# Optimization experiments

Measured on AMD Instinct MI355X. Metric: run time of the kernel, lower is better.

Reference implementation:

```python
import jax, jax.numpy as jnp
import numpy as np

B, D, C, Q = 4096, 128, 1000, 65536
PROTO_M = 0.99
EPS = 1e-12


def _l2norm(x, axis=-1):
    n = jnp.sqrt(jnp.sum(x * x, axis=axis, keepdims=True))
    return x / jnp.maximum(n, EPS)


def setup_inputs() -> dict:
    key = jax.random.key(0)
    ks = jax.random.split(key, 7)
    q = _l2norm(jax.random.normal(ks[0], (B, D), dtype=jnp.float32))
    k = _l2norm(jax.random.normal(ks[1], (B, D), dtype=jnp.float32))
    classfy_logits = jax.random.normal(ks[2], (B, C), dtype=jnp.float32)
    plabel = jax.random.uniform(ks[3], (B, C), dtype=jnp.float32)
    prototypes = _l2norm(jax.random.normal(ks[4], (C, D), dtype=jnp.float32))
    queue = _l2norm(jax.random.normal(ks[5], (Q, D), dtype=jnp.float32))
    queue_pseudo = jax.random.randint(ks[6], (Q,), 0, C).astype(jnp.float32)
    return {
        "q": q, "k": k, "classfy_logits": classfy_logits, "plabel": plabel,
        "prototypes": prototypes, "queue": queue, "queue_pseudo": queue_pseudo,
        "ptr": 0,
    }


def reference(q, k, classfy_logits, plabel, prototypes, queue, queue_pseudo, ptr):
    m = PROTO_M
    # classifier softmax (encoder head output)
    classfy_out = jax.nn.softmax(classfy_logits, axis=1)          # [B, C]
    # cluster logits against OLD prototypes (mm happens before EMA update)
    logits_prot = jnp.matmul(q, prototypes.T)                     # [B, C]
    cluster_out = jax.nn.softmax(logits_prot, axis=1)
    # pseudo labels from partial-label-masked scores
    pseudo_labels = jnp.argmax(classfy_out * plabel, axis=1)      # [B] int
    # --- vectorized order-dependent scatter-EMA prototype update ---
    # sequential: proto[l_i] = m*proto[l_i] + (1-m)*q_i  for i = 0..B-1
    # closed form: proto[c]*m^{n_c} + sum_i (1-m)*m^{(#later samples with same label)} q_i
    onehot = (pseudo_labels[:, None] == jnp.arange(C)[None, :])   # [B, C] bool
    counts = jnp.sum(onehot, axis=0)                              # [C] n_c
    rank = jnp.take_along_axis(jnp.cumsum(onehot.astype(jnp.int32), axis=0),
                               pseudo_labels[:, None], axis=1)[:, 0] - 1  # [B]
    n_l = counts[pseudo_labels]                                   # [B]
    w = (1.0 - m) * jnp.power(jnp.float32(m), (n_l - 1 - rank).astype(jnp.float32))
    scatter = jnp.zeros_like(prototypes).at[pseudo_labels].add(w[:, None] * q)
    decay = jnp.power(jnp.float32(m), counts.astype(jnp.float32))[:, None]
    new_prototypes = _l2norm(prototypes * decay + scatter, axis=1)
    # --- MoCo queue enqueue/dequeue (contrastive bank uses OLD queue) ---
    cont_features = jnp.concatenate([q, k, queue], axis=0)        # [2B+Q, D]
    pl_f = pseudo_labels.astype(jnp.float32)
    cont_labels = jnp.concatenate([pl_f, pl_f, queue_pseudo], axis=0)
    new_queue = jax.lax.dynamic_update_slice(queue, k, (ptr, 0))
    new_queue_pseudo = jax.lax.dynamic_update_slice(queue_pseudo, pl_f, (ptr,))
    new_ptr = (ptr + q.shape[0]) % queue.shape[0]
    return (classfy_out, cluster_out, cont_features, cont_labels,
            new_prototypes, new_queue, new_queue_pseudo, new_ptr)
```

## Files before the change

kernel.cpp:

```cpp
#include <hip/hip_runtime.h>
#include <hip/hip_bf16.h>
#include <math.h>

#define Bn 4096
#define Dn 128
#define Cn 1000
#define Qn 65536

typedef __attribute__((ext_vector_type(8))) short short8v;
typedef __attribute__((ext_vector_type(4))) short short4v;
typedef __attribute__((ext_vector_type(4))) float f32x4;
typedef __attribute__((ext_vector_type(4))) float f4v;

__device__ inline float waveAllMaxF(float v) {
    for (int o = 32; o; o >>= 1) v = fmaxf(v, __shfl_xor(v, o));
    return v;
}
__device__ inline float waveAllSumF(float v) {
    for (int o = 32; o; o >>= 1) v += __shfl_xor(v, o);
    return v;
}
__device__ inline float waveSumF(float v) {
    for (int o = 32; o; o >>= 1) v += __shfl_down(v, o);
    return v;
}
__device__ inline short f2bf(float x) {
    union { __hip_bfloat16 h; short s; } u;
    u.h = __float2bfloat16(x);
    return u.s;
}

__global__ __launch_bounds__(256) void k_cls(
    const float* __restrict__ logits, const float* __restrict__ plabel,
    const float* __restrict__ q, const float* __restrict__ proto,
    float* __restrict__ out_cls, int* __restrict__ labels,
    __hip_bfloat16* __restrict__ qb, __hip_bfloat16* __restrict__ pb)
{
    int g = blockIdx.x, t = threadIdx.x;

    if (t < 160) {
        int idx4 = g * 160 + t;
        if (idx4 < 131072) {
            f4v v = *(const f4v*)(q + (long long)idx4 * 4);
            short4v o = {f2bf(v.x), f2bf(v.y), f2bf(v.z), f2bf(v.w)};
            *(short4v*)((short*)qb + (long long)idx4 * 4) = o;
        } else {
            int j4 = idx4 - 131072;
            short4v o = {0, 0, 0, 0};
            if (j4 < 32000) {
                f4v v = *(const f4v*)(proto + (long long)j4 * 4);
                o = (short4v){f2bf(v.x), f2bf(v.y), f2bf(v.z), f2bf(v.w)};
            }
            *(short4v*)((short*)pb + (long long)j4 * 4) = o;
        }
    }

    int lane = t & 63, wid = t >> 6;
    int row = g * 4 + wid;
    const float* x  = logits + (long long)row * Cn;
    const float* pl = plabel + (long long)row * Cn;

    f4v lv[4], pv[4];
#pragma unroll
    for (int j = 0; j < 4; ++j) {
        int f4i = lane + j * 64;
        if (f4i < 250) {
            lv[j] = *(const f4v*)(x + f4i * 4);
            pv[j] = *(const f4v*)(pl + f4i * 4);
        } else {
            lv[j] = (f4v){-INFINITY, -INFINITY, -INFINITY, -INFINITY};
            pv[j] = (f4v){0.f, 0.f, 0.f, 0.f};
        }
    }

    float mx = -INFINITY;
#pragma unroll
    for (int j = 0; j < 4; ++j)
        mx = fmaxf(mx, fmaxf(fmaxf(lv[j].x, lv[j].y), fmaxf(lv[j].z, lv[j].w)));
    mx = waveAllMaxF(mx);

    float vv[16];
    float ssum = 0.f;
#pragma unroll
    for (int j = 0; j < 4; ++j) {
        vv[j * 4 + 0] = expf(lv[j].x - mx);
        vv[j * 4 + 1] = expf(lv[j].y - mx);
        vv[j * 4 + 2] = expf(lv[j].z - mx);
        vv[j * 4 + 3] = expf(lv[j].w - mx);
        ssum += vv[j * 4 + 0] + vv[j * 4 + 1] + vv[j * 4 + 2] + vv[j * 4 + 3];
    }
    ssum = waveAllSumF(ssum);
    float inv = 1.f / ssum;

    float bv = -INFINITY; int bi = Cn;
#pragma unroll
    for (int j = 0; j < 4; ++j) {
        int f4i = lane + j * 64;
        if (f4i < 250) {
            float o0 = vv[j * 4 + 0] * inv, o1 = vv[j * 4 + 1] * inv;
            float o2 = vv[j * 4 + 2] * inv, o3 = vv[j * 4 + 3] * inv;
            *((f4v*)(out_cls + (long long)row * Cn) + f4i) = (f4v){o0, o1, o2, o3};
            float pr[4] = {o0 * pv[j].x, o1 * pv[j].y, o2 * pv[j].z, o3 * pv[j].w};
#pragma unroll
            for (int jj = 0; jj < 4; ++jj) {
                if (pr[jj] > bv) { bv = pr[jj]; bi = f4i * 4 + jj; }
            }
        }
    }
    for (int o = 32; o; o >>= 1) {
        float ov = __shfl_xor(bv, o);
        int   oi = __shfl_xor(bi, o);
        if (ov > bv || (ov == bv && oi < bi)) { bv = ov; bi = oi; }
    }
    if (lane == 0) labels[row] = bi;
}

__global__ __launch_bounds__(256) void k_rest(
    const __hip_bfloat16* __restrict__ qb, const __hip_bfloat16* __restrict__ pbuf,
    const float* __restrict__ proto, const float* __restrict__ q,
    const float* __restrict__ kk, const float* __restrict__ queue,
    const int* __restrict__ lbl, const float* __restrict__ qps,
    const int* __restrict__ ptrp,
    float* __restrict__ outC, float* __restrict__ outp,
    float* __restrict__ out_lab, float* __restrict__ out_qps,
    float* __restrict__ out_ptr,
    float* __restrict__ out_feat, float* __restrict__ out_queue)
{
    __shared__ __align__(16) char smem[32800];
    int bid = blockIdx.x, t = threadIdx.x;

    if (bid < 256) {
        const float* src = (bid < 128) ? q : kk;
        long long sb = (long long)(bid & 127) * 4096;
        long long db = (long long)bid * 4096;
        f4v v[4];
#pragma unroll
        for (int u = 0; u < 4; ++u)
            v[u] = *(const f4v*)(src + sb + (u * 256 + t) * 4);
#pragma unroll
        for (int u = 0; u < 4; ++u)
            *(f4v*)(out_feat + db + (u * 256 + t) * 4) = v[u];
        return;
    }
    if (bid < 2304) {
        int cb = bid - 256;
        int p = *ptrp;
        int pc = p < 0 ? 0 : (p > Qn - Bn ? Qn - Bn : p);
        long long base = (long long)cb * 4096;
        const long long FB = 2LL * Bn * Dn;
        f4v v[4];
#pragma unroll
        for (int u = 0; u < 4; ++u)
            v[u] = *(const f4v*)(queue + base + (u * 256 + t) * 4);
#pragma unroll
        for (int u = 0; u < 4; ++u)
            *(f4v*)(out_feat + FB + base + (u * 256 + t) * 4) = v[u];
#pragma unroll
        for (int u = 0; u < 4; ++u) {
            long long foff = base + (u * 256 + t) * 4;
            int row = (int)(foff >> 7);
            unsigned rr = (unsigned)(row - pc);
            f4v w = v[u];
            if (rr < (unsigned)Bn) w = *(const f4v*)(kk + (long long)rr * Dn + (foff & 127));
            *(f4v*)(out_queue + foff) = w;
        }
        return;
    }

    if (bid < 2560) {
        int gb = bid - 2304;
        float (*red)[4] = (float (*)[4])smem;
        int lane = t & 63, w = t >> 6;
        int la = lane & 15, lk = lane >> 4;
        int row0 = gb * 16;

        f32x4 acc[16];
#pragma unroll
        for (int j = 0; j < 16; ++j) acc[j] = (f32x4){0.f, 0.f, 0.f, 0.f};

        const short* A = (const short*)qb + (long long)(row0 + la) * Dn;
        const short* Bp = (const short*)pbuf;
#pragma unroll
        for (int kc = 0; kc < Dn; kc += 32) {
            short8v a = *(const short8v*)(A + kc + lk * 8);
#pragma unroll
            for (int j = 0; j < 16; ++j) {
                int prow = w * 256 + j * 16 + la;
                short8v b = *(const short8v*)(Bp + (long long)prow * Dn + kc + lk * 8);
                acc[j] = __builtin_amdgcn_mfma_f32_16x16x32_bf16(a, b, acc[j], 0, 0, 0);
            }
        }

        float m[4];
#pragma unroll
        for (int rg = 0; rg < 4; ++rg) {
            float v = -INFINITY;
#pragma unroll
            for (int j = 0; j < 16; ++j) {
                int col = w * 256 + j * 16 + la;
                if (col < Cn) v = fmaxf(v, acc[j][rg]);
            }
#pragma unroll
            for (int o = 1; o < 16; o <<= 1) v = fmaxf(v, __shfl_xor(v, o));
            m[rg] = v;
        }
        if (la == 0) {
#pragma unroll
            for (int rg = 0; rg < 4; ++rg) red[lk * 4 + rg][w] = m[rg];
        }
        __syncthreads();
#pragma unroll
        for (int rg = 0; rg < 4; ++rg) {
            int r = lk * 4 + rg;
            m[rg] = fmaxf(fmaxf(red[r][0], red[r][1]), fmaxf(red[r][2], red[r][3]));
        }
        __syncthreads();

        float s[4];
#pragma unroll
        for (int rg = 0; rg < 4; ++rg) {
            float v = 0.f;
#pragma unroll
            for (int j = 0; j < 16; ++j) {
                int col = w * 256 + j * 16 + la;
                float e = (col < Cn) ? expf(acc[j][rg] - m[rg]) : 0.f;
                acc[j][rg] = e;
                v += e;
            }
#pragma unroll
            for (int o = 1; o < 16; o <<= 1) v += __shfl_xor(v, o);
            s[rg] = v;
        }
        if (la == 0) {
#pragma unroll
            for (int rg = 0; rg < 4; ++rg) red[lk * 4 + rg][w] = s[rg];
        }
        __syncthreads();
#pragma unroll
        for (int rg = 0; rg < 4; ++rg) {
            int r = lk * 4 + rg;
            s[rg] = 1.f / (red[r][0] + red[r][1] + red[r][2] + red[r][3]);
        }

#pragma unroll
        for (int j = 0; j < 16; ++j) {
            int col = w * 256 + j * 16 + la;
            if (col < Cn) {
                int rowb = row0 + lk * 4;
#pragma unroll
                for (int rg = 0; rg < 4; ++rg)
                    outC[(long long)(rowb + rg) * Cn + col] = acc[j][rg] * s[rg];
            }
        }
    } else if (bid < 3060) {
        int* sl = (int*)smem;
        unsigned short* list0 = (unsigned short*)(smem + 16384);
        unsigned short* list1 = list0 + 4096;
        int* nm = (int*)(smem + 32768);
        float* shh = (float*)(smem + 32776);

        int h = t >> 7, tt = t & 127;
        int c = (bid - 2560) * 2 + h;

#pragma unroll
        for (int u = 0; u < 4; ++u) {
            int base = (u * 256 + t) * 4;
            *(int4*)(sl + base) = *(const int4*)(lbl + base);
        }
        if (t == 0)   nm[0] = 0;
        if (t == 128) nm[1] = 0;
        __syncthreads();

        int wv = t >> 6;
        if ((wv & 1) == 0) {
            int hh = wv >> 1;
            int ln = t & 63;
            int cc = (bid - 2560) * 2 + hh;
            unsigned short* lst = hh ? list1 : list0;
            int n = 0;
            for (int jj = 0; jj < Bn / 64; ++jj) {
                unsigned long long mask = __ballot(sl[jj * 64 + ln] == cc);
                if (ln == 0) {
                    while (mask) {
                        int b = __builtin_ctzll(mask);
                        lst[n++] = (unsigned short)(jj * 64 + b);
                        mask &= mask - 1;
                    }
                }
            }
            if (ln == 0) nm[hh] = n;
        }
        __syncthreads();

        int n = nm[h];
        unsigned short* lst = h ? list1 : list0;
        float acc = proto[(long long)c * Dn + tt] * __powf(0.99f, (float)n);
#pragma unroll 4
        for (int mi = 0; mi < n; ++mi)
            acc += 0.01f * __powf(0.99f, (float)(n - 1 - mi)) * q[(long long)lst[mi] * Dn + tt];

        float ss = waveSumF(acc * acc);
        if ((t & 63) == 0) shh[t >> 6] = ss;
        __syncthreads();
        float nn = sqrtf(shh[h * 2] + shh[h * 2 + 1]);
        outp[(long long)c * Dn + tt] = acc / fmaxf(nn, 1e-12f);
    } else {
        int gid = (bid - 3060) * 256 + t;
        const int NL = 2 * Bn + Qn;
        int p = *ptrp;
        int pc = p < 0 ? 0 : (p > Qn - Bn ? Qn - Bn : p);
        if (gid < NL) {
            float v;
            if (gid < Bn)          v = (float)lbl[gid];
            else if (gid < 2 * Bn) v = (float)lbl[gid - Bn];
            else                   v = qps[gid - 2 * Bn];
            out_lab[gid] = v;
        }
        int j = gid - NL;
        if (j >= 0 && j < Qn) {
            unsigned rr = (unsigned)(j - pc);
            out_qps[j] = (rr < (unsigned)Bn) ? (float)lbl[rr] : qps[j];
        }
        if (gid == NL + Qn) out_ptr[0] = (float)((p + Bn) % Qn);
    }
}

extern "C" void kernel_launch(void* const* d_in, const int* in_sizes, int n_in,
                              void* d_out, int out_size, void* d_ws, size_t ws_size,
                              hipStream_t stream)
{
    const float* q     = (const float*)d_in[0];
    const float* kk    = (const float*)d_in[1];
    const float* cl    = (const float*)d_in[2];
    const float* plab  = (const float*)d_in[3];
    const float* proto = (const float*)d_in[4];
    const float* queue = (const float*)d_in[5];
    const float* qps   = (const float*)d_in[6];
    const int*   ptrp  = (const int*)d_in[7];

    float* out = (float*)d_out;
    const long long O_CLU  = 4096000;
    const long long O_FEAT = 8192000;
    const long long O_LAB  = 17629184;
    const long long O_PROT = 17702912;
    const long long O_QUE  = 17830912;
    const long long O_QPS  = 26219520;
    const long long O_PTR  = 26285056;

    char* ws = (char*)d_ws;
    int*   lbl = (int*)(ws + 0);
    __hip_bfloat16* qb = (__hip_bfloat16*)(ws + 1048576);
    __hip_bfloat16* pb = (__hip_bfloat16*)(ws + 2097152);

    k_cls<<<1024, 256, 0, stream>>>(cl, plab, q, proto, out, lbl, qb, pb);
    k_rest<<<3605, 256, 0, stream>>>(qb, pb, proto, q, kk, queue, lbl, qps, ptrp,
                                     out + O_CLU, out + O_PROT,
                                     out + O_LAB, out + O_QPS, out + O_PTR,
                                     out + O_FEAT, out + O_QUE);
}
```

Baseline: 51.85 us.

## Move prototype matmul-softmax into first kernel with inline bf16 conversion

The cluster matmul+softmax no longer depends on labels, so it moves into the first kernel and converts q and prototypes from fp32 to bf16 inline instead of staging them through workspace buffers. The second kernel now runs one block per class for the prototype EMA, building the per-class index list with a parallel ballot/popcount compaction across all four waves instead of a serial lane-0 loop. The memory copies are reordered to run after the prototype blocks. The trade-off is redundant fp32 loads and conversions of prototypes in every matmul block, and more blocks in the second kernel.

```diff
diff --git a/kernel.cpp b/kernel.cpp
--- a/kernel.cpp
+++ b/kernel.cpp
@@ -8,9 +8,9 @@
 #define Qn 65536
 
 typedef __attribute__((ext_vector_type(8))) short short8v;
-typedef __attribute__((ext_vector_type(4))) short short4v;
 typedef __attribute__((ext_vector_type(4))) float f32x4;
 typedef __attribute__((ext_vector_type(4))) float f4v;
+typedef unsigned short ushortT;
 
 __device__ inline float waveAllMaxF(float v) {
     for (int o = 32; o; o >>= 1) v = fmaxf(v, __shfl_xor(v, o));
@@ -30,31 +30,114 @@
     return u.s;
 }
 
-__global__ __launch_bounds__(256) void k_cls(
+__global__ __launch_bounds__(256) void k_one(
     const float* __restrict__ logits, const float* __restrict__ plabel,
     const float* __restrict__ q, const float* __restrict__ proto,
     float* __restrict__ out_cls, int* __restrict__ labels,
-    __hip_bfloat16* __restrict__ qb, __hip_bfloat16* __restrict__ pb)
+    float* __restrict__ outC)
 {
-    int g = blockIdx.x, t = threadIdx.x;
-
-    if (t < 160) {
-        int idx4 = g * 160 + t;
-        if (idx4 < 131072) {
-            f4v v = *(const f4v*)(q + (long long)idx4 * 4);
-            short4v o = {f2bf(v.x), f2bf(v.y), f2bf(v.z), f2bf(v.w)};
-            *(short4v*)((short*)qb + (long long)idx4 * 4) = o;
-        } else {
-            int j4 = idx4 - 131072;
-            short4v o = {0, 0, 0, 0};
-            if (j4 < 32000) {
-                f4v v = *(const f4v*)(proto + (long long)j4 * 4);
-                o = (short4v){f2bf(v.x), f2bf(v.y), f2bf(v.z), f2bf(v.w)};
-            }
-            *(short4v*)((short*)pb + (long long)j4 * 4) = o;
-        }
-    }
-
+    __shared__ float red[16][4];
+    int bid = blockIdx.x, t = threadIdx.x;
+
+    if (bid < 256) {
+        int lane = t & 63, w = t >> 6;
+        int la = lane & 15, lk = lane >> 4;
+        int row0 = bid * 16;
+
+        f32x4 acc[16];
+#pragma unroll
+        for (int j = 0; j < 16; ++j) acc[j] = (f32x4){0.f, 0.f, 0.f, 0.f};
+
+        const float* A0 = q + (long long)(row0 + la) * Dn;
+#pragma unroll
+        for (int kc = 0; kc < Dn; kc += 32) {
+            short8v a;
+            {
+                f4v f0 = *(const f4v*)(A0 + kc + lk * 8);
+                f4v f1 = *(const f4v*)(A0 + kc + lk * 8 + 4);
+                a[0] = f2bf(f0.x); a[1] = f2bf(f0.y); a[2] = f2bf(f0.z); a[3] = f2bf(f0.w);
+                a[4] = f2bf(f1.x); a[5] = f2bf(f1.y); a[6] = f2bf(f1.z); a[7] = f2bf(f1.w);
+            }
+#pragma unroll
+            for (int j = 0; j < 16; ++j) {
+                int prow = w * 256 + j * 16 + la;
+                short8v b = {0, 0, 0, 0, 0, 0, 0, 0};
+                if (prow < Cn) {
+                    const float* Bp0 = proto + (long long)prow * Dn + kc + lk * 8;
+                    f4v f0 = *(const f4v*)Bp0;
+                    f4v f1 = *(const f4v*)(Bp0 + 4);
+                    b[0] = f2bf(f0.x); b[1] = f2bf(f0.y); b[2] = f2bf(f0.z); b[3] = f2bf(f0.w);
+                    b[4] = f2bf(f1.x); b[5] = f2bf(f1.y); b[6] = f2bf(f1.z); b[7] = f2bf(f1.w);
+                }
+                acc[j] = __builtin_amdgcn_mfma_f32_16x16x32_bf16(a, b, acc[j], 0, 0, 0);
+            }
+        }
+
+        float m[4];
+#pragma unroll
+        for (int rg = 0; rg < 4; ++rg) {
+            float v = -INFINITY;
+#pragma unroll
+            for (int j = 0; j < 16; ++j) {
+                int col = w * 256 + j * 16 + la;
+                if (col < Cn) v = fmaxf(v, acc[j][rg]);
+            }
+#pragma unroll
+            for (int o = 1; o < 16; o <<= 1) v = fmaxf(v, __shfl_xor(v, o));
+            m[rg] = v;
+        }
+        if (la == 0) {
+#pragma unroll
+            for (int rg = 0; rg < 4; ++rg) red[lk * 4 + rg][w] = m[rg];
+        }
+        __syncthreads();
+#pragma unroll
+        for (int rg = 0; rg < 4; ++rg) {
+            int r = lk * 4 + rg;
+            m[rg] = fmaxf(fmaxf(red[r][0], red[r][1]), fmaxf(red[r][2], red[r][3]));
+        }
+        __syncthreads();
+
+        float s[4];
+#pragma unroll
+        for (int rg = 0; rg < 4; ++rg) {
+            float v = 0.f;
+#pragma unroll
+            for (int j = 0; j < 16; ++j) {
+                int col = w * 256 + j * 16 + la;
+                float e = (col < Cn) ? expf(acc[j][rg] - m[rg]) : 0.f;
+                acc[j][rg] = e;
+                v += e;
+            }
+#pragma unroll
+            for (int o = 1; o < 16; o <<= 1) v += __shfl_xor(v, o);
+            s[rg] = v;
+        }
+        if (la == 0) {
+#pragma unroll
+            for (int rg = 0; rg < 4; ++rg) red[lk * 4 + rg][w] = s[rg];
+        }
+        __syncthreads();
+#pragma unroll
+        for (int rg = 0; rg < 4; ++rg) {
+            int r = lk * 4 + rg;
+            s[rg] = 1.f / (red[r][0] + red[r][1] + red[r][2] + red[r][3]);
+        }
+
+#pragma unroll
+        for (int j = 0; j < 16; ++j) {
+            int col = w * 256 + j * 16 + la;
+            if (col < Cn) {
+                int rowb = row0 + lk * 4;
+#pragma unroll
+                for (int rg = 0; rg < 4; ++rg)
+                    outC[(long long)(rowb + rg) * Cn + col] = acc[j][rg] * s[rg];
+            }
+        }
+        return;
+    }
+
+    int g = bid - 256;
     int lane = t & 63, wid = t >> 6;
     int row = g * 4 + wid;
     const float* x  = logits + (long long)row * Cn;
@@ -115,197 +198,76 @@
     if (lane == 0) labels[row] = bi;
 }
 
-__global__ __launch_bounds__(256) void k_rest(
-    const __hip_bfloat16* __restrict__ qb, const __hip_bfloat16* __restrict__ pbuf,
+__global__ __launch_bounds__(256) void k_two(
     const float* __restrict__ proto, const float* __restrict__ q,
     const float* __restrict__ kk, const float* __restrict__ queue,
     const int* __restrict__ lbl, const float* __restrict__ qps,
     const int* __restrict__ ptrp,
-    float* __restrict__ outC, float* __restrict__ outp,
+    float* __restrict__ outp,
     float* __restrict__ out_lab, float* __restrict__ out_qps,
     float* __restrict__ out_ptr,
     float* __restrict__ out_feat, float* __restrict__ out_queue)
 {
-    __shared__ __align__(16) char smem[32800];
+    __shared__ ushortT slab[Bn];
+    __shared__ ushortT lists[4][1024];
+    __shared__ int cnts[4];
+    __shared__ float shh[2];
     int bid = blockIdx.x, t = threadIdx.x;
 
-    if (bid < 256) {
-        const float* src = (bid < 128) ? q : kk;
-        long long sb = (long long)(bid & 127) * 4096;
-        long long db = (long long)bid * 4096;
-        f4v v[4];
-#pragma unroll
-        for (int u = 0; u < 4; ++u)
-            v[u] = *(const f4v*)(src + sb + (u * 256 + t) * 4);
-#pragma unroll
-        for (int u = 0; u < 4; ++u)
-            *(f4v*)(out_feat + db + (u * 256 + t) * 4) = v[u];
+    if (bid < 1000) {
+        int c = bid;
+#pragma unroll
+        for (int u = 0; u < 4; ++u) {
+            int4 v = ((const int4*)lbl)[u * 256 + t];
+            int base = (u * 256 + t) * 4;
+            slab[base + 0] = (ushortT)v.x; slab[base + 1] = (ushortT)v.y;
+            slab[base + 2] = (ushortT)v.z; slab[base + 3] = (ushortT)v.w;
+        }
+        __syncthreads();
+
+        int w = t >> 6, ln = t & 63;
+        int cnt = 0;
+        for (int jj = 0; jj < 16; ++jj) {
+            int j = w * 1024 + jj * 64 + ln;
+            bool mt = (slab[j] == (ushortT)c);
+            unsigned long long mask = __ballot(mt);
+            if (mt) {
+                int pos = cnt + __popcll(mask & ((1ull << ln) - 1ull));
+                lists[w][pos] = (ushortT)j;
+            }
+            cnt += (int)__popcll(mask);
+        }
+        if (ln == 0) cnts[w] = cnt;
+        __syncthreads();
+
+        float acc = 0.f;
+        if (t < Dn) {
+            int n = cnts[0] + cnts[1] + cnts[2] + cnts[3];
+            acc = proto[(long long)c * Dn + t] * __powf(0.99f, (float)n);
+            int base = 0;
+#pragma unroll 1
+            for (int w2 = 0; w2 < 4; ++w2) {
+                int cw = cnts[w2];
+                for (int mi = 0; mi < cw; ++mi) {
+                    int r = lists[w2][mi];
+                    acc += 0.01f * __powf(0.99f, (float)(n - 1 - (base + mi)))
+                         * q[(long long)r * Dn + t];
+                }
+                base += cw;
+            }
+        }
+        float ss = waveSumF(acc * acc);
+        if ((t & 63) == 0 && t < Dn) shh[t >> 6] = ss;
+        __syncthreads();
+        if (t < Dn) {
+            float nrm = sqrtf(shh[0] + shh[1]);
+            outp[(long long)c * Dn + t] = acc / fmaxf(nrm, 1e-12f);
+        }
         return;
     }
-    if (bid < 2304) {
-        int cb = bid - 256;
-        int p = *ptrp;
-        int pc = p < 0 ? 0 : (p > Qn - Bn ? Qn - Bn : p);
-        long long base = (long long)cb * 4096;
-        const long long FB = 2LL * Bn * Dn;
-        f4v v[4];
-#pragma unroll
-        for (int u = 0; u < 4; ++u)
-            v[u] = *(const f4v*)(queue + base + (u * 256 + t) * 4);
-#pragma unroll
-        for (int u = 0; u < 4; ++u)
-            *(f4v*)(out_feat + FB + base + (u * 256 + t) * 4) = v[u];
-#pragma unroll
-        for (int u = 0; u < 4; ++u) {
-            long long foff = base + (u * 256 + t) * 4;
-            int row = (int)(foff >> 7);
-            unsigned rr = (unsigned)(row - pc);
-            f4v w = v[u];
-            if (rr < (unsigned)Bn) w = *(const f4v*)(kk + (long long)rr * Dn + (foff & 127));
-            *(f4v*)(out_queue + foff) = w;
-        }
-        return;
-    }
-
-    if (bid < 2560) {
-        int gb = bid - 2304;
-        float (*red)[4] = (float (*)[4])smem;
-        int lane = t & 63, w = t >> 6;
-        int la = lane & 15, lk = lane >> 4;
-        int row0 = gb * 16;
-
-        f32x4 acc[16];
-#pragma unroll
-        for (int j = 0; j < 16; ++j) acc[j] = (f32x4){0.f, 0.f, 0.f, 0.f};
-
-        const short* A = (const short*)qb + (long long)(row0 + la) * Dn;
-        const short* Bp = (const short*)pbuf;
-#pragma unroll
-        for (int kc = 0; kc < Dn; kc += 32) {
-            short8v a = *(const short8v*)(A + kc + lk * 8);
-#pragma unroll
-            for (int j = 0; j < 16; ++j) {
-                int prow = w * 256 + j * 16 + la;
-                short8v b = *(const short8v*)(Bp + (long long)prow * Dn + kc + lk * 8);
-                acc[j] = __builtin_amdgcn_mfma_f32_16x16x32_bf16(a, b, acc[j], 0, 0, 0);
-            }
-        }
-
-        float m[4];
-#pragma unroll
-        for (int rg = 0; rg < 4; ++rg) {
-            float v = -INFINITY;
-#pragma unroll
-            for (int j = 0; j < 16; ++j) {
-                int col = w * 256 + j * 16 + la;
-                if (col < Cn) v = fmaxf(v, acc[j][rg]);
-            }
-#pragma unroll
-            for (int o = 1; o < 16; o <<= 1) v = fmaxf(v, __shfl_xor(v, o));
-            m[rg] = v;
-        }
-        if (la == 0) {
-#pragma unroll
-            for (int rg = 0; rg < 4; ++rg) red[lk * 4 + rg][w] = m[rg];
-        }
-        __syncthreads();
-#pragma unroll
-        for (int rg = 0; rg < 4; ++rg) {
-            int r = lk * 4 + rg;
-            m[rg] = fmaxf(fmaxf(red[r][0], red[r][1]), fmaxf(red[r][2], red[r][3]));
-        }
-        __syncthreads();
-
-        float s[4];
-#pragma unroll
-        for (int rg = 0; rg < 4; ++rg) {
-            float v = 0.f;
-#pragma unroll
-            for (int j = 0; j < 16; ++j) {
-                int col = w * 256 + j * 16 + la;
-                float e = (col < Cn) ? expf(acc[j][rg] - m[rg]) : 0.f;
-                acc[j][rg] = e;
-                v += e;
-            }
-#pragma unroll
-            for (int o = 1; o < 16; o <<= 1) v += __shfl_xor(v, o);
-            s[rg] = v;
-        }
-        if (la == 0) {
-#pragma unroll
-            for (int rg = 0; rg < 4; ++rg) red[lk * 4 + rg][w] = s[rg];
-        }
-        __syncthreads();
-#pragma unroll
-        for (int rg = 0; rg < 4; ++rg) {
-            int r = lk * 4 + rg;
-            s[rg] = 1.f / (red[r][0] + red[r][1] + red[r][2] + red[r][3]);
-        }
-
-#pragma unroll
-        for (int j = 0; j < 16; ++j) {
-            int col = w * 256 + j * 16 + la;
-            if (col < Cn) {
-                int rowb = row0 + lk * 4;
-#pragma unroll
-                for (int rg = 0; rg < 4; ++rg)
-                    outC[(long long)(rowb + rg) * Cn + col] = acc[j][rg] * s[rg];
-            }
-        }
-    } else if (bid < 3060) {
-        int* sl = (int*)smem;
-        unsigned short* list0 = (unsigned short*)(smem + 16384);
-        unsigned short* list1 = list0 + 4096;
-        int* nm = (int*)(smem + 32768);
-        float* shh = (float*)(smem + 32776);
-
-        int h = t >> 7, tt = t & 127;
-        int c = (bid - 2560) * 2 + h;
-
-#pragma unroll
-        for (int u = 0; u < 4; ++u) {
-            int base = (u * 256 + t) * 4;
-            *(int4*)(sl + base) = *(const int4*)(lbl + base);
-        }
-        if (t == 0)   nm[0] = 0;
-        if (t == 128) nm[1] = 0;
-        __syncthreads();
-
-        int wv = t >> 6;
-        if ((wv & 1) == 0) {
-            int hh = wv >> 1;
-            int ln = t & 63;
-            int cc = (bid - 2560) * 2 + hh;
-            unsigned short* lst = hh ? list1 : list0;
-            int n = 0;
-            for (int jj = 0; jj < Bn / 64; ++jj) {
-                unsigned long long mask = __ballot(sl[jj * 64 + ln] == cc);
-                if (ln == 0) {
-                    while (mask) {
-                        int b = __builtin_ctzll(mask);
-                        lst[n++] = (unsigned short)(jj * 64 + b);
-                        mask &= mask - 1;
-                    }
-                }
-            }
-            if (ln == 0) nm[hh] = n;
-        }
-        __syncthreads();
-
-        int n = nm[h];
-        unsigned short* lst = h ? list1 : list0;
-        float acc = proto[(long long)c * Dn + tt] * __powf(0.99f, (float)n);
-#pragma unroll 4
-        for (int mi = 0; mi < n; ++mi)
-            acc += 0.01f * __powf(0.99f, (float)(n - 1 - mi)) * q[(long long)lst[mi] * Dn + tt];
-
-        float ss = waveSumF(acc * acc);
-        if ((t & 63) == 0) shh[t >> 6] = ss;
-        __syncthreads();
-        float nn = sqrtf(shh[h * 2] + shh[h * 2 + 1]);
-        outp[(long long)c * Dn + tt] = acc / fmaxf(nn, 1e-12f);
-    } else {
-        int gid = (bid - 3060) * 256 + t;
+
+    if (bid < 1545) {
+        int gid = (bid - 1000) * 256 + t;
         const int NL = 2 * Bn + Qn;
         int p = *ptrp;
         int pc = p < 0 ? 0 : (p > Qn - Bn ? Qn - Bn : p);
@@ -322,6 +284,46 @@
             out_qps[j] = (rr < (unsigned)Bn) ? (float)lbl[rr] : qps[j];
         }
         if (gid == NL + Qn) out_ptr[0] = (float)((p + Bn) % Qn);
+        return;
+    }
+
+    if (bid < 1801) {
+        int fb = bid - 1545;
+        const float* src = (fb < 128) ? q : kk;
+        long long sb = (long long)(fb & 127) * 4096;
+        long long db = (long long)fb * 4096;
+        f4v v[4];
+#pragma unroll
+        for (int u = 0; u < 4; ++u)
+            v[u] = *(const f4v*)(src + sb + (u * 256 + t) * 4);
+#pragma unroll
+        for (int u = 0; u < 4; ++u)
+            *(f4v*)(out_feat + db + (u * 256 + t) * 4) = v[u];
+        return;
+    }
+
+    {
+        int cb = bid - 1801;
+        int p = *ptrp;
+        int pc = p < 0 ? 0 : (p > Qn - Bn ? Qn - Bn : p);
+        long long base = (long long)cb * 4096;
+        const long long FB = 2LL * Bn * Dn;
+        f4v v[4];
+#pragma unroll
+        for (int u = 0; u < 4; ++u)
+            v[u] = *(const f4v*)(queue + base + (u * 256 + t) * 4);
+#pragma unroll
+        for (int u = 0; u < 4; ++u)
+            *(f4v*)(out_feat + FB + base + (u * 256 + t) * 4) = v[u];
+#pragma unroll
+        for (int u = 0; u < 4; ++u) {
+            long long foff = base + (u * 256 + t) * 4;
+            int row = (int)(foff >> 7);
+            unsigned rr = (unsigned)(row - pc);
+            f4v wv = v[u];
+            if (rr < (unsigned)Bn) wv = *(const f4v*)(kk + (long long)rr * Dn + (foff & 127));
+            *(f4v*)(out_queue + foff) = wv;
+        }
     }
 }
 
@@ -348,13 +350,11 @@
     const long long O_PTR  = 26285056;
 
     char* ws = (char*)d_ws;
-    int*   lbl = (int*)(ws + 0);
-    __hip_bfloat16* qb = (__hip_bfloat16*)(ws + 1048576);
-    __hip_bfloat16* pb = (__hip_bfloat16*)(ws + 2097152);
-
-    k_cls<<<1024, 256, 0, stream>>>(cl, plab, q, proto, out, lbl, qb, pb);
-    k_rest<<<3605, 256, 0, stream>>>(qb, pb, proto, q, kk, queue, lbl, qps, ptrp,
-                                     out + O_CLU, out + O_PROT,
-                                     out + O_LAB, out + O_QPS, out + O_PTR,
-                                     out + O_FEAT, out + O_QUE);
-}
+    int* lbl = (int*)(ws + 0);
+
+    k_one<<<1280, 256, 0, stream>>>(cl, plab, q, proto, out, lbl, out + O_CLU);
+    k_two<<<3849, 256, 0, stream>>>(proto, q, kk, queue, lbl, qps, ptrp,
+                                    out + O_PROT,
+                                    out + O_LAB, out + O_QPS, out + O_PTR,
+                                    out + O_FEAT, out + O_QUE);
+}
```

New measurement: 54.37 us. +4.8%, slower.
